# Optimization experiments

Measured on AMD Instinct MI355X. Metric: run time of the kernel, lower is better.

## Reference

```python
import jax, jax.numpy as jnp
import numpy as np

H = 8        # num_heads
D = 64       # qkv_dim
E = 512      # embed_dim = H*D
MS = 16      # ms_hidden_dim


def setup_inputs() -> dict:
    key = jax.random.key(0)
    ks = jax.random.split(key, 12)
    b, r, c = 4, 512, 512
    row_emb = jax.random.normal(ks[0], (b, r, E), dtype=jnp.float32)
    col_emb = jax.random.normal(ks[1], (b, c, E), dtype=jnp.float32)
    cost_mat = jax.random.uniform(ks[2], (b, r, c), dtype=jnp.float32)
    attn_mask = jax.random.randint(ks[3], (b, H, r, c), 0, 2) > 0
    s = 1.0 / np.sqrt(E)
    Wq = jax.random.uniform(ks[4], (H * D, E), minval=-s, maxval=s)
    Wk = jax.random.uniform(ks[5], (H * D, E), minval=-s, maxval=s)
    Wv = jax.random.uniform(ks[6], (H * D, E), minval=-s, maxval=s)
    Wout = jax.random.uniform(ks[7], (E, E), minval=-s, maxval=s)
    m1 = np.sqrt(0.5)
    m2 = np.sqrt(1.0 / MS)
    Wmix1 = jax.random.uniform(ks[8], (H * MS, 2 * H), minval=-m1, maxval=m1)
    Wmix2 = jax.random.uniform(ks[9], (H, H * MS), minval=-m2, maxval=m2)
    return {"row_emb": row_emb, "col_emb": col_emb, "cost_mat": cost_mat,
            "attn_mask": attn_mask, "Wq": Wq, "Wk": Wk, "Wv": Wv,
            "Wmix1": Wmix1, "Wmix2": Wmix2, "Wout": Wout}


def reference(row_emb, col_emb, cost_mat, attn_mask, Wq, Wk, Wv, Wmix1, Wmix2, Wout):
    b, r, _ = row_emb.shape
    c = col_emb.shape[1]
    norm = 1.0 / jnp.sqrt(jnp.asarray(D, row_emb.dtype))
    # projections -> [b, h, s, d]
    q = (row_emb @ Wq.T).reshape(b, r, H, D).transpose(0, 2, 1, 3)
    k = (col_emb @ Wk.T).reshape(b, c, H, D).transpose(0, 2, 1, 3)
    v = (col_emb @ Wv.T).reshape(b, c, H, D).transpose(0, 2, 1, 3)
    dot = norm * jnp.einsum('bhrd,bhcd->bhrc', q, k)            # [b,h,r,c]
    cost = jnp.broadcast_to(cost_mat[:, None, :, :], dot.shape)  # [b,h,r,c]
    # stack then rearrange 'b h r c s -> b r c (h s)' (h major, s minor)
    two = jnp.stack([dot, cost], axis=-1)                        # [b,h,r,c,2]
    two = two.transpose(0, 2, 3, 1, 4).reshape(b, r, c, 2 * H)
    hid = jax.nn.relu(two @ Wmix1.T)                             # [b,r,c,H*MS]
    ms = hid @ Wmix2.T                                           # [b,r,c,H]
    logits = ms.transpose(0, 3, 1, 2)                            # [b,h,r,c]
    # mask handling: rows that are fully masked become fully unmasked
    all_masked = jnp.all(attn_mask, axis=-1, keepdims=True)
    mask = jnp.where(all_masked, False, attn_mask)
    logits = jnp.where(mask, -jnp.inf, logits)
    weights = jax.nn.softmax(logits, axis=-1)
    out = jnp.einsum('bhrc,bhcd->bhrd', weights, v)              # [b,h,r,d]
    out = out.transpose(0, 2, 1, 3).reshape(b, r, H * D)         # b s (h d)
    return out @ Wout.T
```

## Files before the change

### kernel.cpp

```cpp
#include <hip/hip_runtime.h>
#include <math.h>

typedef __attribute__((ext_vector_type(8))) short bf16x8;
typedef __attribute__((ext_vector_type(4))) float f32x4;
typedef unsigned short ushort_t;

static __device__ inline unsigned short f2bf(float f) {
    union { float f; unsigned u; } v; v.f = f;
    unsigned r = v.u + 0x7fff + ((v.u >> 16) & 1);
    return (unsigned short)(r >> 16);
}

#if defined(__has_builtin)
#  if __has_builtin(__builtin_amdgcn_cvt_pk_bf16_f32)
#    define HAVE_PK_BF16 1
#  endif
#endif

static __device__ inline unsigned pk2bf(float a, float b) {
#ifdef HAVE_PK_BF16
    auto r = __builtin_amdgcn_cvt_pk_bf16_f32(a, b);
    unsigned u; __builtin_memcpy(&u, &r, 4);
    return u;
#else
    return (unsigned)f2bf(a) | ((unsigned)f2bf(b) << 16);
#endif
}

static __device__ inline bf16x8 ld8f32_bf16(const float* __restrict__ p) {
    const float4 v0 = *(const float4*)p;
    const float4 v1 = *(const float4*)(p + 4);
    union { unsigned u[4]; bf16x8 v; } t;
    t.u[0] = pk2bf(v0.x, v0.y); t.u[1] = pk2bf(v0.z, v0.w);
    t.u[2] = pk2bf(v1.x, v1.y); t.u[3] = pk2bf(v1.z, v1.w);
    return t.v;
}

__global__ __launch_bounds__(256) void gemm_qkv(const float* __restrict__ rowe,
                                                const float* __restrict__ cole,
                                                const float* __restrict__ Wq,
                                                const float* __restrict__ Wk,
                                                const float* __restrict__ Wv,
                                                ushort_t* __restrict__ Qb,
                                                ushort_t* __restrict__ Kb,
                                                ushort_t* __restrict__ Vt) {
    const int z = blockIdx.z;
    const float* A = (z == 0) ? rowe : cole;
    const float* B = (z == 0) ? Wq : (z == 1) ? Wk : Wv;

    const int t    = threadIdx.x;
    const int w    = t >> 6;
    const int lane = t & 63;
    const int quad = lane >> 4;
    const int sl   = lane & 15;
    const int m0 = blockIdx.x * 64 + (w >> 1) * 32;
    const int n0 = blockIdx.y * 64 + (w & 1) * 32;

    f32x4 acc[2][2] = {};

    for (int k0 = 0; k0 < 512; k0 += 32) {
        bf16x8 a[2], b[2];
#pragma unroll
        for (int rs = 0; rs < 2; ++rs)
            a[rs] = ld8f32_bf16(A + (size_t)(m0 + rs * 16 + sl) * 512 + k0 + quad * 8);
#pragma unroll
        for (int cs = 0; cs < 2; ++cs)
            b[cs] = ld8f32_bf16(B + (size_t)(n0 + cs * 16 + sl) * 512 + k0 + quad * 8);
#pragma unroll
        for (int rs = 0; rs < 2; ++rs)
#pragma unroll
            for (int cs = 0; cs < 2; ++cs)
                acc[rs][cs] = __builtin_amdgcn_mfma_f32_16x16x32_bf16(a[rs], b[cs], acc[rs][cs], 0, 0, 0);
    }

#pragma unroll
    for (int rs = 0; rs < 2; ++rs)
#pragma unroll
        for (int cs = 0; cs < 2; ++cs) {
            const int n = n0 + cs * 16 + sl;
            if (z == 2) {
                const int mb   = m0 + rs * 16 + quad * 4;
                const int bidx = mb >> 9, c = mb & 511;
                const int h = n >> 6, d = n & 63;
                ushort4 o;
                o.x = f2bf(acc[rs][cs][0]); o.y = f2bf(acc[rs][cs][1]);
                o.z = f2bf(acc[rs][cs][2]); o.w = f2bf(acc[rs][cs][3]);
                *(ushort4*)(Vt + (size_t)(((bidx * 8 + h) * 64 + d)) * 512 + c) = o;
            } else {
                ushort_t* C = (z == 0) ? Qb : Kb;
#pragma unroll
                for (int reg = 0; reg < 4; ++reg) {
                    const int m = m0 + rs * 16 + quad * 4 + reg;
                    C[(size_t)m * 512 + n] = f2bf(acc[rs][cs][reg]);
                }
            }
        }
}

__global__ __launch_bounds__(256) void gemm_out(const ushort_t* __restrict__ A,
                                                const float* __restrict__ B,
                                                float* __restrict__ C) {
    const int t    = threadIdx.x;
    const int w    = t >> 6;
    const int lane = t & 63;
    const int quad = lane >> 4;
    const int sl   = lane & 15;
    const int m0 = blockIdx.x * 64 + (w >> 1) * 32;
    const int n0 = blockIdx.y * 64 + (w & 1) * 32;

    f32x4 acc[2][2] = {};

    for (int k0 = 0; k0 < 512; k0 += 32) {
        bf16x8 a[2], b[2];
#pragma unroll
        for (int rs = 0; rs < 2; ++rs)
            a[rs] = *(const bf16x8*)(A + (size_t)(m0 + rs * 16 + sl) * 512 + k0 + quad * 8);
#pragma unroll
        for (int cs = 0; cs < 2; ++cs)
            b[cs] = ld8f32_bf16(B + (size_t)(n0 + cs * 16 + sl) * 512 + k0 + quad * 8);
#pragma unroll
        for (int rs = 0; rs < 2; ++rs)
#pragma unroll
            for (int cs = 0; cs < 2; ++cs)
                acc[rs][cs] = __builtin_amdgcn_mfma_f32_16x16x32_bf16(a[rs], b[cs], acc[rs][cs], 0, 0, 0);
    }

#pragma unroll
    for (int rs = 0; rs < 2; ++rs)
#pragma unroll
        for (int cs = 0; cs < 2; ++cs) {
            const int n = n0 + cs * 16 + sl;
#pragma unroll
            for (int reg = 0; reg < 4; ++reg) {
                const int m = m0 + rs * 16 + quad * 4 + reg;
                C[(size_t)m * 512 + n] = acc[rs][cs][reg];
            }
        }
}

__global__ __launch_bounds__(512) void dot_mlp_v5(const ushort_t* __restrict__ Qb,
                                                  const ushort_t* __restrict__ Kb,
                                                  const float* __restrict__ cost,
                                                  const float* __restrict__ W1,
                                                  const float* __restrict__ W2,
                                                  float* __restrict__ logits) {
    __shared__ ushort_t Xs[1024 * 18];
    __shared__ ushort_t hidS[8 * 16 * 36];
    __shared__ ushort_t W1fs[128 * 16];
    __shared__ ushort_t W2ss[8 * 128];

    const int b  = blockIdx.z;
    const int r0 = blockIdx.y * 32;
    const int c0 = blockIdx.x * 32;
    const int t    = threadIdx.x;
    const int w    = t >> 6;
    const int lane = t & 63;
    const int quad = lane >> 4;
    const int sl   = lane & 15;

    const bf16x8 zf = {0, 0, 0, 0, 0, 0, 0, 0};

    if (t < 128) {
        float s = 0.f;
#pragma unroll
        for (int h = 0; h < 8; ++h) {
            W1fs[t * 16 + h] = f2bf(W1[t * 16 + 2 * h]);
            s += W1[t * 16 + 2 * h + 1];
        }
        W1fs[t * 16 + 8] = f2bf(s);
#pragma unroll
        for (int k = 9; k < 16; ++k) W1fs[t * 16 + k] = 0;
    }
#pragma unroll
    for (int i = 0; i < 2; ++i) W2ss[t + i * 512] = f2bf(W2[t + i * 512]);

#pragma unroll
    for (int i = 0; i < 2; ++i) {
        const int cell = t + i * 512;
        const int rl = cell >> 5, cl = cell & 31;
        unsigned* base = (unsigned*)(Xs + cell * 18 + 8);
        base[0] = (unsigned)f2bf(cost[((size_t)b * 512 + r0 + rl) * 512 + c0 + cl]);
        base[1] = 0; base[2] = 0; base[3] = 0; base[4] = 0;
    }

    {
        const int hp = w & 3;
        const int h0 = hp * 2;
        const int rs = w >> 2;
        bf16x8 af[2][2], bfr[2][2][2];
#pragma unroll
        for (int hh = 0; hh < 2; ++hh)
#pragma unroll
            for (int ks = 0; ks < 2; ++ks) {
                af[hh][ks] = *(const bf16x8*)(Qb +
                    ((size_t)(b * 512 + r0 + rs * 16 + sl) * 512 + (h0 + hh) * 64 + ks * 32 + quad * 8));
#pragma unroll
                for (int cs = 0; cs < 2; ++cs)
                    bfr[hh][cs][ks] = *(const bf16x8*)(Kb +
                        ((size_t)(b * 512 + c0 + cs * 16 + sl) * 512 + (h0 + hh) * 64 + ks * 32 + quad * 8));
            }
        f32x4 dacc[2][2];
#pragma unroll
        for (int hh = 0; hh < 2; ++hh)
#pragma unroll
            for (int cs = 0; cs < 2; ++cs) {
                f32x4 acc = {0.f, 0.f, 0.f, 0.f};
                acc = __builtin_amdgcn_mfma_f32_16x16x32_bf16(af[hh][0], bfr[hh][cs][0], acc, 0, 0, 0);
                acc = __builtin_amdgcn_mfma_f32_16x16x32_bf16(af[hh][1], bfr[hh][cs][1], acc, 0, 0, 0);
                dacc[hh][cs] = acc;
            }
#pragma unroll
        for (int cs = 0; cs < 2; ++cs)
#pragma unroll
            for (int reg = 0; reg < 4; ++reg) {
                const int cell = (rs * 16 + quad * 4 + reg) * 32 + cs * 16 + sl;
                ((unsigned*)Xs)[cell * 9 + hp] =
                    pk2bf(dacc[0][cs][reg] * 0.125f, dacc[1][cs][reg] * 0.125f);
            }
    }

    __syncthreads();

    bf16x8 bw1[8];
#pragma unroll
    for (int nt = 0; nt < 8; ++nt)
        bw1[nt] = (quad < 2) ? *(const bf16x8*)&W1fs[(nt * 16 + sl) * 16 + quad * 8] : zf;
    bf16x8 bw2[4];
#pragma unroll
    for (int ks = 0; ks < 4; ++ks) {
        union { ushort_t s[8]; bf16x8 v; } tu;
#pragma unroll
        for (int i = 0; i < 8; ++i) {
            const int p  = quad * 8 + i;
            const int jc = (p >> 1) | ((p & 1) << 4);
            tu.s[i] = (sl < 8) ? W2ss[sl * 128 + ks * 32 + jc] : (ushort_t)0;
        }
        bw2[ks] = tu.v;
    }

    ushort_t* hidW = hidS + w * (16 * 36);

#pragma unroll
    for (int mt = 0; mt < 8; ++mt) {
        const int gmt = w * 8 + mt;
        const int cb  = gmt * 16;

        bf16x8 a1 = zf;
        if (quad < 2) {
            const unsigned* xr = (const unsigned*)Xs + (size_t)(cb + sl) * 9 + quad * 4;
            union { unsigned u[4]; bf16x8 v; } tmp;
            tmp.u[0] = xr[0]; tmp.u[1] = xr[1]; tmp.u[2] = xr[2]; tmp.u[3] = xr[3];
            a1 = tmp.v;
        }

        f32x4 acc2 = {0.f, 0.f, 0.f, 0.f};
#pragma unroll
        for (int ks = 0; ks < 4; ++ks) {
            f32x4 z = {0.f, 0.f, 0.f, 0.f};
            const f32x4 h0 = __builtin_amdgcn_mfma_f32_16x16x32_bf16(a1, bw1[2 * ks],     z, 0, 0, 0);
            const f32x4 h1 = __builtin_amdgcn_mfma_f32_16x16x32_bf16(a1, bw1[2 * ks + 1], z, 0, 0, 0);
#pragma unroll
            for (int rp = 0; rp < 4; ++rp)
                ((unsigned*)hidW)[(quad * 4 + rp) * 18 + sl] =
                    pk2bf(fmaxf(h0[rp], 0.f), fmaxf(h1[rp], 0.f));
            union { uint2 u2[2]; bf16x8 v; } tu;
            const ushort_t* hp2 = hidW + sl * 36 + quad * 8;
            tu.u2[0] = *(const uint2*)hp2;
            tu.u2[1] = *(const uint2*)(hp2 + 4);
            acc2 = __builtin_amdgcn_mfma_f32_16x16x32_bf16(tu.v, bw2[ks], acc2, 0, 0, 0);
        }

        if (sl < 8) {
            const int r = r0 + (gmt >> 1);
            const int cbase = c0 + (gmt & 1) * 16 + quad * 4;
            float4 o; o.x = acc2[0]; o.y = acc2[1]; o.z = acc2[2]; o.w = acc2[3];
            *(float4*)&logits[((size_t)(b * 8 + sl) * 512 + r) * 512 + cbase] = o;
        }
    }
}

__global__ __launch_bounds__(256) void softmax_pv(const float* __restrict__ logits,
                                                  const int* __restrict__ mask,
                                                  const ushort_t* __restrict__ Vt,
                                                  ushort_t* __restrict__ Aout) {
    __shared__ ushort_t Ps[16 * 520];

    const int t    = threadIdx.x;
    const int w    = t >> 6;
    const int lane = t & 63;
    const int quad = lane >> 4;
    const int sl   = lane & 15;
    const int rt = blockIdx.x;
    const int bh = blockIdx.y;
    const int r0 = rt * 16;

#pragma unroll
    for (int rr = 0; rr < 4; ++rr) {
        const int row = w * 4 + rr;
        const float* lp = logits + ((size_t)bh * 512 + r0 + row) * 512;
        const int*   mp = mask   + ((size_t)bh * 512 + r0 + row) * 512;

        float v[8]; int m[8]; int allm = 1;
#pragma unroll
        for (int i = 0; i < 8; ++i) {
            v[i] = lp[lane + i * 64];
            m[i] = mp[lane + i * 64];
            allm &= (m[i] != 0);
        }
        const bool all_masked = (__all(allm) != 0);

        float mx = -__builtin_inff();
#pragma unroll
        for (int i = 0; i < 8; ++i) {
            const bool keep = all_masked || (m[i] == 0);
            if (keep) mx = fmaxf(mx, v[i]);
        }
#pragma unroll
        for (int s = 32; s > 0; s >>= 1) mx = fmaxf(mx, __shfl_xor(mx, s, 64));

        float e[8]; float sum = 0.f;
#pragma unroll
        for (int i = 0; i < 8; ++i) {
            const bool keep = all_masked || (m[i] == 0);
            e[i] = keep ? __expf(v[i] - mx) : 0.f;
            sum += e[i];
        }
#pragma unroll
        for (int s = 32; s > 0; s >>= 1) sum += __shfl_xor(sum, s, 64);

        const float inv = 1.f / sum;
#pragma unroll
        for (int i = 0; i < 8; ++i)
            Ps[row * 520 + lane + i * 64] = f2bf(e[i] * inv);
    }

    __syncthreads();

    const int n0w = w * 16;
    const ushort_t* vb = Vt + (size_t)bh * 64 * 512;

    f32x4 acc = {0.f, 0.f, 0.f, 0.f};
    for (int ks = 0; ks < 16; ++ks) {
        union { uint2 u2[2]; bf16x8 v; } ta;
        const ushort_t* pp = Ps + (size_t)sl * 520 + ks * 32 + quad * 8;
        ta.u2[0] = *(const uint2*)pp;
        ta.u2[1] = *(const uint2*)(pp + 4);
        const bf16x8 bv = *(const bf16x8*)(vb + (size_t)(n0w + sl) * 512 + ks * 32 + quad * 8);
        acc = __builtin_amdgcn_mfma_f32_16x16x32_bf16(ta.v, bv, acc, 0, 0, 0);
    }

    const int bidx = bh >> 3, h = bh & 7;
    ushort_t* Cb = Aout + (size_t)bidx * 512 * 512 + h * 64;
    const int n = n0w + sl;
#pragma unroll
    for (int reg = 0; reg < 4; ++reg) {
        const int m = r0 + quad * 4 + reg;
        Cb[(size_t)m * 512 + n] = f2bf(acc[reg]);
    }
}

extern "C" void kernel_launch(void* const* d_in, const int* in_sizes, int n_in,
                              void* d_out, int out_size, void* d_ws, size_t ws_size,
                              hipStream_t stream) {
    const float* row_emb = (const float*)d_in[0];
    const float* col_emb = (const float*)d_in[1];
    const float* cost    = (const float*)d_in[2];
    const int*   mask    = (const int*)d_in[3];
    const float* Wq      = (const float*)d_in[4];
    const float* Wk      = (const float*)d_in[5];
    const float* Wv      = (const float*)d_in[6];
    const float* Wmix1   = (const float*)d_in[7];
    const float* Wmix2   = (const float*)d_in[8];
    const float* Wout    = (const float*)d_in[9];
    float* out = (float*)d_out;

    char* ws = (char*)d_ws;
    const size_t MB = (size_t)1 << 20;
    ushort_t* Qb    = (ushort_t*)(ws);
    ushort_t* Kb    = (ushort_t*)(ws + 2 * MB);
    ushort_t* Vt    = (ushort_t*)(ws + 4 * MB);
    ushort_t* Aoutb = (ushort_t*)(ws + 6 * MB);
    float* logitsBuf = (float*)(ws + 8 * MB);

    gemm_qkv<<<dim3(32, 8, 3), 256, 0, stream>>>(row_emb, col_emb, Wq, Wk, Wv, Qb, Kb, Vt);

    dot_mlp_v5<<<dim3(16, 16, 4), 512, 0, stream>>>(Qb, Kb, cost, Wmix1, Wmix2, logitsBuf);

    softmax_pv<<<dim3(32, 32), 256, 0, stream>>>(logitsBuf, mask, Vt, Aoutb);

    gemm_out<<<dim3(32, 8), 256, 0, stream>>>(Aoutb, Wout, out);
}
```

Measured before the change: 219.0 us.

## Pre-convert fp32 inputs and weights to bf16, software-pipeline GEMM loads

Adds a single conversion kernel that turns row/col embeddings and all four weight matrices into bf16 in workspace once, so the QKV and output GEMMs load half the bytes and skip per-tile fp32-to-bf16 packing. Both GEMM loops are rewritten to prefetch the next K-slice into registers while the current MFMAs run. The cost is an extra kernel launch plus a full read/write pass over about 3M elements, and the workspace layout grows and shifts.

```diff
diff --git a/kernel.cpp b/kernel.cpp
--- a/kernel.cpp
+++ b/kernel.cpp
@@ -27,26 +27,37 @@
 #endif
 }
 
-static __device__ inline bf16x8 ld8f32_bf16(const float* __restrict__ p) {
-    const float4 v0 = *(const float4*)p;
-    const float4 v1 = *(const float4*)(p + 4);
-    union { unsigned u[4]; bf16x8 v; } t;
-    t.u[0] = pk2bf(v0.x, v0.y); t.u[1] = pk2bf(v0.z, v0.w);
-    t.u[2] = pk2bf(v1.x, v1.y); t.u[3] = pk2bf(v1.z, v1.w);
-    return t.v;
-}
-
-__global__ __launch_bounds__(256) void gemm_qkv(const float* __restrict__ rowe,
-                                                const float* __restrict__ cole,
-                                                const float* __restrict__ Wq,
-                                                const float* __restrict__ Wk,
-                                                const float* __restrict__ Wv,
+__global__ __launch_bounds__(256) void convert_all(const float* __restrict__ a0,
+                                                   const float* __restrict__ a1,
+                                                   const float* __restrict__ a2,
+                                                   const float* __restrict__ a3,
+                                                   const float* __restrict__ a4,
+                                                   const float* __restrict__ a5,
+                                                   ushort_t* __restrict__ dst) {
+    const size_t e = ((size_t)blockIdx.x * 256 + threadIdx.x) * 4;
+    const float* src; size_t off;
+    if      (e < 1048576) { src = a0; off = 0; }
+    else if (e < 2097152) { src = a1; off = 1048576; }
+    else if (e < 2359296) { src = a2; off = 2097152; }
+    else if (e < 2621440) { src = a3; off = 2359296; }
+    else if (e < 2883584) { src = a4; off = 2621440; }
+    else                  { src = a5; off = 2883584; }
+    const float4 v = *(const float4*)(src + (e - off));
+    uint2 o; o.x = pk2bf(v.x, v.y); o.y = pk2bf(v.z, v.w);
+    *(uint2*)(dst + e) = o;
+}
+
+__global__ __launch_bounds__(256) void gemm_qkv(const ushort_t* __restrict__ rowb,
+                                                const ushort_t* __restrict__ colb,
+                                                const ushort_t* __restrict__ Wqb,
+                                                const ushort_t* __restrict__ Wkb,
+                                                const ushort_t* __restrict__ Wvb,
                                                 ushort_t* __restrict__ Qb,
                                                 ushort_t* __restrict__ Kb,
                                                 ushort_t* __restrict__ Vt) {
     const int z = blockIdx.z;
-    const float* A = (z == 0) ? rowe : cole;
-    const float* B = (z == 0) ? Wq : (z == 1) ? Wk : Wv;
+    const ushort_t* A = (z == 0) ? rowb : colb;
+    const ushort_t* B = (z == 0) ? Wqb : (z == 1) ? Wkb : Wvb;
 
     const int t    = threadIdx.x;
     const int w    = t >> 6;
@@ -56,21 +67,32 @@
     const int m0 = blockIdx.x * 64 + (w >> 1) * 32;
     const int n0 = blockIdx.y * 64 + (w & 1) * 32;
 
+    const ushort_t* ap0 = A + (size_t)(m0 + sl) * 512 + quad * 8;
+    const ushort_t* ap1 = A + (size_t)(m0 + 16 + sl) * 512 + quad * 8;
+    const ushort_t* bp0 = B + (size_t)(n0 + sl) * 512 + quad * 8;
+    const ushort_t* bp1 = B + (size_t)(n0 + 16 + sl) * 512 + quad * 8;
+
     f32x4 acc[2][2] = {};
 
-    for (int k0 = 0; k0 < 512; k0 += 32) {
-        bf16x8 a[2], b[2];
-#pragma unroll
-        for (int rs = 0; rs < 2; ++rs)
-            a[rs] = ld8f32_bf16(A + (size_t)(m0 + rs * 16 + sl) * 512 + k0 + quad * 8);
-#pragma unroll
-        for (int cs = 0; cs < 2; ++cs)
-            b[cs] = ld8f32_bf16(B + (size_t)(n0 + cs * 16 + sl) * 512 + k0 + quad * 8);
-#pragma unroll
-        for (int rs = 0; rs < 2; ++rs)
-#pragma unroll
-            for (int cs = 0; cs < 2; ++cs)
-                acc[rs][cs] = __builtin_amdgcn_mfma_f32_16x16x32_bf16(a[rs], b[cs], acc[rs][cs], 0, 0, 0);
+    bf16x8 a0 = *(const bf16x8*)ap0;
+    bf16x8 a1 = *(const bf16x8*)ap1;
+    bf16x8 b0 = *(const bf16x8*)bp0;
+    bf16x8 b1 = *(const bf16x8*)bp1;
+
+    for (int ks = 0; ks < 16; ++ks) {
+        bf16x8 na0, na1, nb0, nb1;
+        if (ks < 15) {
+            const int k0 = (ks + 1) * 32;
+            na0 = *(const bf16x8*)(ap0 + k0);
+            na1 = *(const bf16x8*)(ap1 + k0);
+            nb0 = *(const bf16x8*)(bp0 + k0);
+            nb1 = *(const bf16x8*)(bp1 + k0);
+        }
+        acc[0][0] = __builtin_amdgcn_mfma_f32_16x16x32_bf16(a0, b0, acc[0][0], 0, 0, 0);
+        acc[0][1] = __builtin_amdgcn_mfma_f32_16x16x32_bf16(a0, b1, acc[0][1], 0, 0, 0);
+        acc[1][0] = __builtin_amdgcn_mfma_f32_16x16x32_bf16(a1, b0, acc[1][0], 0, 0, 0);
+        acc[1][1] = __builtin_amdgcn_mfma_f32_16x16x32_bf16(a1, b1, acc[1][1], 0, 0, 0);
+        a0 = na0; a1 = na1; b0 = nb0; b1 = nb1;
     }
 
 #pragma unroll
@@ -98,7 +120,7 @@
 }
 
 __global__ __launch_bounds__(256) void gemm_out(const ushort_t* __restrict__ A,
-                                                const float* __restrict__ B,
+                                                const ushort_t* __restrict__ B,
                                                 float* __restrict__ C) {
     const int t    = threadIdx.x;
     const int w    = t >> 6;
@@ -108,21 +130,32 @@
     const int m0 = blockIdx.x * 64 + (w >> 1) * 32;
     const int n0 = blockIdx.y * 64 + (w & 1) * 32;
 
+    const ushort_t* ap0 = A + (size_t)(m0 + sl) * 512 + quad * 8;
+    const ushort_t* ap1 = A + (size_t)(m0 + 16 + sl) * 512 + quad * 8;
+    const ushort_t* bp0 = B + (size_t)(n0 + sl) * 512 + quad * 8;
+    const ushort_t* bp1 = B + (size_t)(n0 + 16 + sl) * 512 + quad * 8;
+
     f32x4 acc[2][2] = {};
 
-    for (int k0 = 0; k0 < 512; k0 += 32) {
-        bf16x8 a[2], b[2];
-#pragma unroll
-        for (int rs = 0; rs < 2; ++rs)
-            a[rs] = *(const bf16x8*)(A + (size_t)(m0 + rs * 16 + sl) * 512 + k0 + quad * 8);
-#pragma unroll
-        for (int cs = 0; cs < 2; ++cs)
-            b[cs] = ld8f32_bf16(B + (size_t)(n0 + cs * 16 + sl) * 512 + k0 + quad * 8);
-#pragma unroll
-        for (int rs = 0; rs < 2; ++rs)
-#pragma unroll
-            for (int cs = 0; cs < 2; ++cs)
-                acc[rs][cs] = __builtin_amdgcn_mfma_f32_16x16x32_bf16(a[rs], b[cs], acc[rs][cs], 0, 0, 0);
+    bf16x8 a0 = *(const bf16x8*)ap0;
+    bf16x8 a1 = *(const bf16x8*)ap1;
+    bf16x8 b0 = *(const bf16x8*)bp0;
+    bf16x8 b1 = *(const bf16x8*)bp1;
+
+    for (int ks = 0; ks < 16; ++ks) {
+        bf16x8 na0, na1, nb0, nb1;
+        if (ks < 15) {
+            const int k0 = (ks + 1) * 32;
+            na0 = *(const bf16x8*)(ap0 + k0);
+            na1 = *(const bf16x8*)(ap1 + k0);
+            nb0 = *(const bf16x8*)(bp0 + k0);
+            nb1 = *(const bf16x8*)(bp1 + k0);
+        }
+        acc[0][0] = __builtin_amdgcn_mfma_f32_16x16x32_bf16(a0, b0, acc[0][0], 0, 0, 0);
+        acc[0][1] = __builtin_amdgcn_mfma_f32_16x16x32_bf16(a0, b1, acc[0][1], 0, 0, 0);
+        acc[1][0] = __builtin_amdgcn_mfma_f32_16x16x32_bf16(a1, b0, acc[1][0], 0, 0, 0);
+        acc[1][1] = __builtin_amdgcn_mfma_f32_16x16x32_bf16(a1, b1, acc[1][1], 0, 0, 0);
+        a0 = na0; a1 = na1; b0 = nb0; b1 = nb1;
     }
 
 #pragma unroll
@@ -376,17 +409,26 @@
 
     char* ws = (char*)d_ws;
     const size_t MB = (size_t)1 << 20;
-    ushort_t* Qb    = (ushort_t*)(ws);
-    ushort_t* Kb    = (ushort_t*)(ws + 2 * MB);
-    ushort_t* Vt    = (ushort_t*)(ws + 4 * MB);
-    ushort_t* Aoutb = (ushort_t*)(ws + 6 * MB);
-    float* logitsBuf = (float*)(ws + 8 * MB);
-
-    gemm_qkv<<<dim3(32, 8, 3), 256, 0, stream>>>(row_emb, col_emb, Wq, Wk, Wv, Qb, Kb, Vt);
+    ushort_t* convDst = (ushort_t*)ws;
+    ushort_t* rowb  = (ushort_t*)(ws);
+    ushort_t* colb  = (ushort_t*)(ws + 2 * MB);
+    ushort_t* Wqb   = (ushort_t*)(ws + 4 * MB);
+    ushort_t* Wkb   = (ushort_t*)(ws + 4 * MB + 512 * 1024);
+    ushort_t* Wvb   = (ushort_t*)(ws + 5 * MB);
+    ushort_t* Woutb = (ushort_t*)(ws + 5 * MB + 512 * 1024);
+    ushort_t* Qb    = (ushort_t*)(ws + 6 * MB);
+    ushort_t* Kb    = (ushort_t*)(ws + 8 * MB);
+    ushort_t* Vt    = (ushort_t*)(ws + 10 * MB);
+    ushort_t* Aoutb = (ushort_t*)(ws + 12 * MB);
+    float* logitsBuf = (float*)(ws + 16 * MB);
+
+    convert_all<<<3072, 256, 0, stream>>>(row_emb, col_emb, Wq, Wk, Wv, Wout, convDst);
+
+    gemm_qkv<<<dim3(32, 8, 3), 256, 0, stream>>>(rowb, colb, Wqb, Wkb, Wvb, Qb, Kb, Vt);
 
     dot_mlp_v5<<<dim3(16, 16, 4), 512, 0, stream>>>(Qb, Kb, cost, Wmix1, Wmix2, logitsBuf);
 
     softmax_pv<<<dim3(32, 32), 256, 0, stream>>>(logitsBuf, mask, Vt, Aoutb);
 
-    gemm_out<<<dim3(32, 8), 256, 0, stream>>>(Aoutb, Wout, out);
-}
+    gemm_out<<<dim3(32, 8), 256, 0, stream>>>(Aoutb, Woutb, out);
+}
```

New measurement: 190.6 us. -13.0%, faster.
